# Performance work log

Measured on AMD Instinct MI355X. Metric: run time of the kernel, lower is better.

The kernel has to match this reference:

```python
import jax, jax.numpy as jnp
import numpy as np

N = 50000      # nodes
E = 400000     # edges
HID = 128      # hidden_size
L = 3          # num_att_layer
K = 9          # rbf_size
H = 4          # heads
C = HID // H   # out_channels per head (32)
G = 512        # graphs in batch
CUTOFF = 10.0


def _rbf(D):
    # ExponentialRBF: softplus(softplus_inverse(x)) == x, so centers/widths are the raw values
    centers = jnp.linspace(1.0, float(np.exp(-CUTOFF)), K)          # (K,)
    width = (0.5 / ((1.0 - np.exp(-CUTOFF)) / K)) ** 2              # scalar
    x = D / CUTOFF
    x3 = x ** 3
    x4 = x3 * x
    x5 = x4 * x
    cut = jnp.where(x < 1.0, 1.0 - 6.0 * x5 + 15.0 * x4 - 10.0 * x3, 0.0)
    return cut[:, None] * jnp.exp(-width * (jnp.exp(-D)[:, None] - centers) ** 2)  # (E,K)


def _ln(x, g, b):
    mu = jnp.mean(x, axis=-1, keepdims=True)
    var = jnp.var(x, axis=-1, keepdims=True)
    return (x - mu) / jnp.sqrt(var + 1e-5) * g + b


def _seg_softmax(logits, seg, n):
    # numerically stable softmax over edges grouped by target node
    m = jax.ops.segment_max(logits, seg, num_segments=n)
    e = jnp.exp(logits - m[seg])
    s = jax.ops.segment_sum(e, seg, num_segments=n)
    return e / s[seg]


def setup_inputs() -> dict:
    key = jax.random.key(0)
    ks = jax.random.split(key, 32)
    s = 1.0 / np.sqrt(HID)
    se = 1.0 / np.sqrt(K + 1)
    sb = 1.0 / np.sqrt(3 * HID)
    nrm = jax.random.normal
    inp = {
        "h": nrm(ks[0], (N, HID), jnp.float32),
        "pos": nrm(ks[1], (N, 3), jnp.float32) * 3.0,
        "edge_weight": jax.random.uniform(ks[2], (E,), jnp.float32),
        "Wq": nrm(ks[3], (L, HID, HID)) * s,   "bq": nrm(ks[4], (L, HID)) * 0.01,
        "Wk": nrm(ks[5], (L, HID, HID)) * s,   "bk": nrm(ks[6], (L, HID)) * 0.01,
        "Wv": nrm(ks[7], (L, HID, HID)) * s,   "bv": nrm(ks[8], (L, HID)) * 0.01,
        "We": nrm(ks[9], (L, K + 1, HID)) * se,
        "Wskip": nrm(ks[10], (L, HID, HID)) * s, "bskip": nrm(ks[11], (L, HID)) * 0.01,
        "Wbeta": nrm(ks[12], (L, 3 * HID, 1)) * sb,
        "Wffn1": nrm(ks[13], (L, HID, HID)) * s, "bffn1": nrm(ks[14], (L, HID)) * 0.01,
        "Wffn2": nrm(ks[15], (L, HID, HID)) * s, "bffn2": nrm(ks[16], (L, HID)) * 0.01,
        "Wffn3": nrm(ks[17], (L, HID, HID)) * s, "bffn3": nrm(ks[18], (L, HID)) * 0.01,
        "ln_g": jnp.ones((HID,), jnp.float32),
        "ln_b": jnp.zeros((HID,), jnp.float32),
        "Wo1": nrm(ks[19], (HID, HID)) * s, "bo1": nrm(ks[20], (HID,)) * 0.01,
        "Wo2": nrm(ks[21], (HID, 1)) * s,   "bo2": nrm(ks[22], (1,)) * 0.01,
        "edge_index": jax.random.randint(ks[23], (2, E), 0, N),
        "batch": jnp.sort(jax.random.randint(ks[24], (N,), 0, G)),
    }
    return inp


def reference(h, pos, edge_weight, Wq, bq, Wk, bk, Wv, bv, We, Wskip, bskip, Wbeta,
              Wffn1, bffn1, Wffn2, bffn2, Wffn3, bffn3, ln_g, ln_b, Wo1, bo1, Wo2, bo2,
              edge_index, batch):
    sp = jax.nn.softplus
    n = h.shape[0]
    src, dst = edge_index[0], edge_index[1]  # source j -> target i
    D = jnp.linalg.norm(pos[dst] - pos[src], axis=-1)              # (E,)
    efeat = jnp.concatenate([_rbf(D), edge_weight[:, None]], -1)   # (E, K+1)
    inv_sqrt_c = 1.0 / np.sqrt(C)

    for i in range(L):
        hn = _ln(h, ln_g, ln_b)
        q = (hn @ Wq[i] + bq[i]).reshape(n, H, C)
        k = (hn @ Wk[i] + bk[i]).reshape(n, H, C)
        v = (hn @ Wv[i] + bv[i]).reshape(n, H, C)
        ea = (efeat @ We[i]).reshape(-1, H, C)                     # (E,H,C)
        kj = k[src] + ea
        alpha = jnp.einsum('ehc,ehc->eh', q[dst], kj) * inv_sqrt_c  # (E,H)
        alpha = _seg_softmax(alpha, dst, n)
        # dropout p=0.5 is a no-op in eval mode
        msg = (v[src] + ea) * alpha[:, :, None]
        out = jax.ops.segment_sum(msg, dst, num_segments=n).reshape(n, H * C)
        x_r = hn @ Wskip[i] + bskip[i]
        beta = jax.nn.sigmoid(jnp.concatenate([out, x_r, out - x_r], -1) @ Wbeta[i])
        out = beta * x_r + (1.0 - beta) * out
        h = hn + sp(out)
        hn2 = _ln(h, ln_g, ln_b)
        f = sp(hn2 @ Wffn1[i] + bffn1[i])
        f = sp(f @ Wffn2[i] + bffn2[i])
        f = sp(f @ Wffn3[i] + bffn3[i])
        h = hn2 + f

    pooled = jax.ops.segment_sum(h, batch, num_segments=G)          # (G, HID)
    return sp(pooled @ Wo1 + bo1) @ Wo2 + bo2                       # (G, 1)
```

## Files before the change

### kernel.cpp

```cpp
#include <hip/hip_runtime.h>
#include <hip/hip_bf16.h>
#include <math.h>

#define HID 128
#define KRBF 9
#define NLAYER 3
#define QWCOLS 640

typedef __attribute__((ext_vector_type(8))) short bf16x8;
typedef __attribute__((ext_vector_type(4))) float f32x4;

__device__ __forceinline__ float sp_(float x){ return fmaxf(x,0.f) + log1pf(expf(-fabsf(x))); }
__device__ __forceinline__ float sigm_(float x){ return 1.f/(1.f+expf(-x)); }
__device__ __forceinline__ float b2f(short s){
  union{unsigned u; float f;} x; x.u = ((unsigned)(unsigned short)s)<<16; return x.f;
}
__device__ __forceinline__ short f2bs(float x){
  __hip_bfloat16 b = __float2bfloat16(x);
  return *reinterpret_cast<short*>(&b);
}
__device__ __forceinline__ float wsum64(float v){
  #pragma unroll
  for(int m=1;m<64;m<<=1) v += __shfl_xor(v,m,64);
  return v;
}
__device__ __forceinline__ float wsum16(float v){
  #pragma unroll
  for(int m=1;m<16;m<<=1) v += __shfl_xor(v,m,64);
  return v;
}
__device__ __forceinline__ int lb_(const int* __restrict__ a, int n, int key){
  int lo=0, hi=n;
  while(lo<hi){ int mid=(lo+hi)>>1; if(a[mid]<key) lo=mid+1; else hi=mid; }
  return lo;
}

__global__ void count_dst(const int* __restrict__ ei, int* __restrict__ counts, int E){
  int e = blockIdx.x*256+threadIdx.x;
  if(e<E) atomicAdd(&counts[ei[E+e]],1);
}
__global__ void scan1(const int* __restrict__ counts, int* __restrict__ tmp,
                      int* __restrict__ bsums, int N){
  __shared__ int lds[256];
  int t = threadIdx.x; int idx = blockIdx.x*256+t;
  int v = (idx<N)? counts[idx]:0;
  lds[t]=v; __syncthreads();
  for(int off=1;off<256;off<<=1){
    int x = (t>=off)? lds[t-off]:0;
    __syncthreads();
    lds[t]+=x; __syncthreads();
  }
  if(idx<N) tmp[idx]=lds[t];
  if(t==255) bsums[blockIdx.x]=lds[255];
}
__global__ void scan2(const int* __restrict__ bsums, int* __restrict__ boffs, int nb){
  __shared__ int lds[256];
  int t=threadIdx.x;
  int v = (t<nb)? bsums[t]:0;
  lds[t]=v; __syncthreads();
  for(int off=1;off<256;off<<=1){
    int x=(t>=off)?lds[t-off]:0;
    __syncthreads();
    lds[t]+=x; __syncthreads();
  }
  if(t<nb) boffs[t] = lds[t]-v;
}
__global__ void finalize_rs(const int* __restrict__ tmp, const int* __restrict__ boffs,
                            int* __restrict__ row_start, int N){
  int idx = blockIdx.x*256+threadIdx.x;
  if(idx<N) row_start[idx+1] = tmp[idx] + boffs[idx>>8];
  if(idx==0) row_start[0]=0;
}
__global__ void csr_scatter(const int* __restrict__ ei, const int* __restrict__ rowst,
                            int* __restrict__ counts2, int* __restrict__ csr, int E){
  int e = blockIdx.x*256+threadIdx.x;
  if(e>=E) return;
  int d = ei[E+e];
  int p = rowst[d] + atomicAdd(&counts2[d],1);
  csr[p] = e;
}
__global__ void sort_seg(const int* __restrict__ rowst, int* __restrict__ csr, int N){
  int n = blockIdx.x*256+threadIdx.x;
  if(n>=N) return;
  int lo=rowst[n], hi=rowst[n+1];
  for(int i=lo+1;i<hi;i++){
    int v=csr[i]; int j=i-1;
    while(j>=lo && csr[j]>v){ csr[j+1]=csr[j]; j--; }
    csr[j+1]=v;
  }
}
__global__ void edge_feat(const float* __restrict__ pos, const float* __restrict__ ew,
                          const int* __restrict__ ei, const int* __restrict__ csr,
                          float* __restrict__ efs, int* __restrict__ esrc, int E){
  int p = blockIdx.x*256 + threadIdx.x;
  if(p>=E) return;
  int e = csr[p];
  int s = ei[e], d = ei[E+e];
  float dx = pos[d*3+0]-pos[s*3+0];
  float dy = pos[d*3+1]-pos[s*3+1];
  float dz = pos[d*3+2]-pos[s*3+2];
  float D = sqrtf(dx*dx+dy*dy+dz*dz);
  float x = D*0.1f;
  float cut = 0.f;
  if(x < 1.f){ float x3=x*x*x, x4=x3*x, x5=x4*x; cut = 1.f - 6.f*x5 + 15.f*x4 - 10.f*x3; }
  float ed = expf(-D);
  const double e10 = 4.5399929762484854e-05;
  const float step  = (float)((e10 - 1.0)/8.0);
  const float width = (float)((4.5/(1.0-e10))*(4.5/(1.0-e10)));
  float r12[12];
  #pragma unroll
  for(int k=0;k<KRBF;k++){
    float c = 1.0f + k*step;
    float dd = ed - c;
    r12[k] = cut*expf(-width*dd*dd);
  }
  r12[9] = ew[e]; r12[10]=0.f; r12[11]=0.f;
  float* o = efs + (size_t)p*12;
  *(float4*)&o[0] = *(float4*)&r12[0];
  *(float4*)&o[4] = *(float4*)&r12[4];
  *(float4*)&o[8] = *(float4*)&r12[8];
  esrc[p] = s;
}

__global__ void pack_w(const float* __restrict__ Wq, const float* __restrict__ Wk,
                       const float* __restrict__ Wv, const float* __restrict__ Wsk,
                       const float* __restrict__ bq, const float* __restrict__ bk,
                       const float* __restrict__ bv, const float* __restrict__ bsk,
                       const float* __restrict__ We,
                       const float* __restrict__ W1, const float* __restrict__ W2,
                       const float* __restrict__ W3,
                       __hip_bfloat16* __restrict__ Wqkvs, float* __restrict__ bqkvs,
                       __hip_bfloat16* __restrict__ Wffn){
  int idx = blockIdx.x*256 + threadIdx.x;
  const int QT = NLAYER*QWCOLS*128;
  const int FT = NLAYER*3*128*128;
  const int BT = NLAYER*QWCOLS;
  if(idx < QT){
    int l = idx / (QWCOLS*128);
    int rem = idx - l*(QWCOLS*128);
    int colp = rem >> 7, k = rem & 127;
    int b = colp >> 7, p = colp & 127;
    int g = ((p&15)<<3) + (p>>4);
    int gcol = b*128 + g;
    float v = 0.f;
    if(gcol < 512){
      const float* src = (gcol<128)?Wq:((gcol<256)?Wk:((gcol<384)?Wv:Wsk));
      v = src[(size_t)l*16384 + k*128 + (gcol&127)];
    } else if(gcol < 552){
      int j = gcol-512; int h=j/10; int r=j-10*h;
      const float* wq = Wq + (size_t)l*16384 + k*128;
      const float* we = We + (size_t)l*1280 + r*128;
      float acc=0.f;
      #pragma unroll 8
      for(int c=32*h;c<32*h+32;c++) acc = fmaf(wq[c], we[c], acc);
      v = acc;
    }
    Wqkvs[idx] = __float2bfloat16(v);
  } else if(idx < QT+FT){
    int j = idx - QT;
    int k = j & 127; int colp = (j>>7)&127; int f = (j>>14)%3; int l = j/(3*16384);
    int g = ((colp&15)<<3) + (colp>>4);
    const float* src = (f==0)?W1:((f==1)?W2:W3);
    Wffn[j] = __float2bfloat16(src[(size_t)l*16384 + k*128 + g]);
  } else if(idx < QT+FT+BT){
    int j = idx - QT - FT;
    int l = j/QWCOLS; int col = j - l*QWCOLS;
    float v = 0.f;
    if(col<512){
      const float* src = (col<128)?bq:((col<256)?bk:((col<384)?bv:bsk));
      v = src[l*128 + (col&127)];
    } else if(col<552){
      int jj=col-512; int h=jj/10; int r=jj-10*h;
      const float* bqp = bq + l*128;
      const float* we = We + (size_t)l*1280 + r*128;
      float acc=0.f;
      for(int c=32*h;c<32*h+32;c++) acc = fmaf(bqp[c], we[c], acc);
      v = acc;
    }
    bqkvs[j] = v;
  }
}

__global__ void ln_node(const float* __restrict__ h, const float* __restrict__ g,
                        const float* __restrict__ b, __hip_bfloat16* __restrict__ hn, int N){
  int n = blockIdx.x*4 + (threadIdx.x>>6);
  if(n>=N) return;
  int lane = threadIdx.x & 63;
  int c = 2*lane;
  float2 v = *(const float2*)&h[(size_t)n*HID + c];
  float s1 = wsum64(v.x+v.y);
  float s2 = wsum64(v.x*v.x+v.y*v.y);
  float mu = s1*(1.f/HID);
  float var = s2*(1.f/HID) - mu*mu;
  float rs = rsqrtf(var + 1e-5f);
  __hip_bfloat162 o;
  o.x = __float2bfloat16((v.x-mu)*rs*g[c]   + b[c]);
  o.y = __float2bfloat16((v.y-mu)*rs*g[c+1] + b[c+1]);
  *(__hip_bfloat162*)&hn[(size_t)n*HID + c] = o;
}

__global__ __launch_bounds__(256) void gemm_qkvs(
    const __hip_bfloat16* __restrict__ A, const __hip_bfloat16* __restrict__ Wt,
    const float* __restrict__ bias,
    __hip_bfloat16* __restrict__ qsO, __hip_bfloat16* __restrict__ kvO,
    float* __restrict__ qwO, int N){
  __shared__ __hip_bfloat16 Ws[128][140];
  int row0 = blockIdx.y*128;
  int cb = blockIdx.x;
  int tid = threadIdx.x;
  {
    int chunk = tid&15, rbase = tid>>4;
    #pragma unroll
    for(int i=0;i<8;i++){
      int p = rbase + 16*i;
      *(float4*)&Ws[p][chunk*8] =
        *(const float4*)&Wt[(size_t)(cb*128+p)*128 + chunk*8];
    }
  }
  int lane = tid&63;
  int m0 = (tid>>6)*32;
  int ql = lane>>4, il = lane&15;
  bf16x8 af[2][4];
  #pragma unroll
  for(int mi=0;mi<2;mi++){
    int r = row0 + m0 + mi*16 + il;
    r = (r < N) ? r : (N-1);
    const __hip_bfloat16* ap = A + (size_t)r*128 + ql*8;
    #pragma unroll
    for(int kc=0;kc<4;kc++) af[mi][kc] = *(const bf16x8*)(ap + kc*32);
  }
  __syncthreads();
  f32x4 acc[2][8];
  #pragma unroll
  for(int mi=0;mi<2;mi++)
    #pragma unroll
    for(int nj=0;nj<8;nj++) acc[mi][nj] = (f32x4){0.f,0.f,0.f,0.f};
  #pragma unroll
  for(int kc=0;kc<4;kc++){
    #pragma unroll
    for(int nj=0;nj<8;nj++){
      bf16x8 bb = *(bf16x8*)&Ws[nj*16+il][kc*32+ql*8];
      #pragma unroll
      for(int mi=0;mi<2;mi++)
        acc[mi][nj] = __builtin_amdgcn_mfma_f32_16x16x32_bf16(af[mi][kc], bb, acc[mi][nj], 0,0,0);
    }
  }
  float bl8[8];
  {
    float4 b0 = *(const float4*)&bias[cb*128 + il*8];
    float4 b1 = *(const float4*)&bias[cb*128 + il*8 + 4];
    bl8[0]=b0.x; bl8[1]=b0.y; bl8[2]=b0.z; bl8[3]=b0.w;
    bl8[4]=b1.x; bl8[5]=b1.y; bl8[6]=b1.z; bl8[7]=b1.w;
  }
  #pragma unroll
  for(int mi=0;mi<2;mi++){
    #pragma unroll
    for(int r=0;r<4;r++){
      int rr = row0 + m0 + mi*16 + ql*4 + r;
      if(rr >= N) continue;
      if(cb < 4){
        bf16x8 o;
        #pragma unroll
        for(int nj=0;nj<8;nj++) o[nj] = f2bs(acc[mi][nj][r] + bl8[nj]);
        __hip_bfloat16* dst;
        if(cb==0)      dst = qsO + (size_t)rr*256 + il*8;
        else if(cb==1) dst = kvO + (size_t)rr*256 + il*8;
        else if(cb==2) dst = kvO + (size_t)rr*256 + 128 + il*8;
        else           dst = qsO + (size_t)rr*256 + 128 + il*8;
        *(bf16x8*)dst = o;
      } else if(il < 5){
        #pragma unroll
        for(int nj=0;nj<8;nj++){
          int g = il*8 + nj;
          int h = g/10, rb = g - 10*h;
          qwO[(size_t)rr*48 + h*12 + rb] = acc[mi][nj][r] + bl8[nj];
        }
      }
    }
  }
}

__global__ __launch_bounds__(256) void attn_fused4(
    const __hip_bfloat16* __restrict__ qs, const __hip_bfloat16* __restrict__ kvb,
    const float* __restrict__ qwb, const float* __restrict__ efs,
    const int* __restrict__ esrc, const float* __restrict__ WeL,
    const int* __restrict__ rowst, const __hip_bfloat16* __restrict__ hn,
    const float* __restrict__ Wb, const float* __restrict__ lng,
    const float* __restrict__ lnb, __hip_bfloat16* __restrict__ hn2, int N){
  int n = blockIdx.x*4 + (threadIdx.x>>6);
  if(n>=N) return;
  int lane = threadIdx.x & 63;
  int eg = lane>>4, sl = lane&15;
  int c8 = sl*8, hd = sl>>2;
  const __hip_bfloat16* rowq = qs + (size_t)n*256;
  float q8[8];
  {
    bf16x8 qv = *(const bf16x8*)&rowq[c8];
    #pragma unroll
    for(int j=0;j<8;j++) q8[j] = b2f(qv[j]);
  }
  const float* qwp = qwb + (size_t)n*48 + hd*12;
  float4 qa = *(const float4*)qwp;
  float4 qb = *(const float4*)(qwp+4);
  float2 qc = *(const float2*)(qwp+8);
  float QW[10] = {qa.x,qa.y,qa.z,qa.w,qb.x,qb.y,qb.z,qb.w,qc.x,qc.y};
  int lo = rowst[n], hi = rowst[n+1];
  float ssum = 0.f, a8[8], S[10];
  #pragma unroll
  for(int j=0;j<8;j++) a8[j]=0.f;
  #pragma unroll
  for(int r=0;r<10;r++) S[r]=0.f;
  int i = lo + eg;
  if(i < hi){
    int s = esrc[i];
    const __hip_bfloat16* kr = kvb + (size_t)s*256;
    bf16x8 kc = *(const bf16x8*)&kr[c8];
    bf16x8 vc = *(const bf16x8*)&kr[128 + c8];
    const float* ef = efs + (size_t)i*12;
    float4 e0 = *(const float4*)&ef[0];
    float4 e1 = *(const float4*)&ef[4];
    float2 e2 = *(const float2*)&ef[8];
    while(true){
      int inext = i + 4;
      bool more = inext < hi;
      bf16x8 kn = kc, vn = vc;
      float4 f0 = e0, f1 = e1; float2 f2 = e2;
      if(more){
        int s2 = esrc[inext];
        const __hip_bfloat16* kr2 = kvb + (size_t)s2*256;
        kn = *(const bf16x8*)&kr2[c8];
        vn = *(const bf16x8*)&kr2[128 + c8];
        const float* ef2 = efs + (size_t)inext*12;
        f0 = *(const float4*)&ef2[0];
        f1 = *(const float4*)&ef2[4];
        f2 = *(const float2*)&ef2[8];
      }
      float d = 0.f;
      #pragma unroll
      for(int j=0;j<8;j++) d = fmaf(q8[j], b2f(kc[j]), d);
      d += __shfl_xor(d,1,64); d += __shfl_xor(d,2,64);
      float lg = d;
      lg = fmaf(e0.x,QW[0],lg); lg = fmaf(e0.y,QW[1],lg);
      lg = fmaf(e0.z,QW[2],lg); lg = fmaf(e0.w,QW[3],lg);
      lg = fmaf(e1.x,QW[4],lg); lg = fmaf(e1.y,QW[5],lg);
      lg = fmaf(e1.z,QW[6],lg); lg = fmaf(e1.w,QW[7],lg);
      lg = fmaf(e2.x,QW[8],lg); lg = fmaf(e2.y,QW[9],lg);
      lg *= 0.17677669529663687f;
      lg = fminf(lg, 80.f);
      float w = __expf(lg);
      ssum += w;
      #pragma unroll
      for(int j=0;j<8;j++) a8[j] = fmaf(w, b2f(vc[j]), a8[j]);
      S[0]=fmaf(w,e0.x,S[0]); S[1]=fmaf(w,e0.y,S[1]); S[2]=fmaf(w,e0.z,S[2]);
      S[3]=fmaf(w,e0.w,S[3]); S[4]=fmaf(w,e1.x,S[4]); S[5]=fmaf(w,e1.y,S[5]);
      S[6]=fmaf(w,e1.z,S[6]); S[7]=fmaf(w,e1.w,S[7]); S[8]=fmaf(w,e2.x,S[8]);
      S[9]=fmaf(w,e2.y,S[9]);
      if(!more) break;
      kc = kn; vc = vn; e0 = f0; e1 = f1; e2 = f2;
      i = inext;
    }
  }
  #pragma unroll
  for(int m=16;m<64;m<<=1){
    ssum += __shfl_xor(ssum,m,64);
    #pragma unroll
    for(int j=0;j<8;j++) a8[j] += __shfl_xor(a8[j],m,64);
    #pragma unroll
    for(int r=0;r<10;r++) S[r] += __shfl_xor(S[r],m,64);
  }
  float inv = (hi>lo)? 1.f/ssum : 0.f;
  float o8[8];
  #pragma unroll
  for(int j=0;j<8;j++) o8[j]=a8[j];
  #pragma unroll
  for(int r=0;r<10;r++){
    float s=S[r];
    float4 wa = *(const float4*)&WeL[r*128+c8];
    float4 wb = *(const float4*)&WeL[r*128+c8+4];
    o8[0]=fmaf(s,wa.x,o8[0]); o8[1]=fmaf(s,wa.y,o8[1]);
    o8[2]=fmaf(s,wa.z,o8[2]); o8[3]=fmaf(s,wa.w,o8[3]);
    o8[4]=fmaf(s,wb.x,o8[4]); o8[5]=fmaf(s,wb.y,o8[5]);
    o8[6]=fmaf(s,wb.z,o8[6]); o8[7]=fmaf(s,wb.w,o8[7]);
  }
  #pragma unroll
  for(int j=0;j<8;j++) o8[j] *= inv;
  float xr8[8];
  {
    bf16x8 xv = *(const bf16x8*)&rowq[128 + c8];
    #pragma unroll
    for(int j=0;j<8;j++) xr8[j] = b2f(xv[j]);
  }
  float wb0[8], wb1[8], wb2[8];
  {
    float4 a0=*(const float4*)&Wb[c8],     a1=*(const float4*)&Wb[c8+4];
    float4 b0=*(const float4*)&Wb[128+c8], b1=*(const float4*)&Wb[128+c8+4];
    float4 c0=*(const float4*)&Wb[256+c8], c1=*(const float4*)&Wb[256+c8+4];
    wb0[0]=a0.x;wb0[1]=a0.y;wb0[2]=a0.z;wb0[3]=a0.w;wb0[4]=a1.x;wb0[5]=a1.y;wb0[6]=a1.z;wb0[7]=a1.w;
    wb1[0]=b0.x;wb1[1]=b0.y;wb1[2]=b0.z;wb1[3]=b0.w;wb1[4]=b1.x;wb1[5]=b1.y;wb1[6]=b1.z;wb1[7]=b1.w;
    wb2[0]=c0.x;wb2[1]=c0.y;wb2[2]=c0.z;wb2[3]=c0.w;wb2[4]=c1.x;wb2[5]=c1.y;wb2[6]=c1.z;wb2[7]=c1.w;
  }
  float pb = 0.f;
  #pragma unroll
  for(int j=0;j<8;j++)
    pb += o8[j]*wb0[j] + xr8[j]*wb1[j] + (o8[j]-xr8[j])*wb2[j];
  pb = wsum16(pb);
  float beta = sigm_(pb);
  float h8[8], s1=0.f, s2=0.f;
  {
    bf16x8 hv = *(const bf16x8*)&hn[(size_t)n*128 + c8];
    #pragma unroll
    for(int j=0;j<8;j++){
      float u = beta*xr8[j] + (1.f-beta)*o8[j];
      float x = b2f(hv[j]) + sp_(u);
      h8[j]=x; s1+=x; s2+=x*x;
    }
  }
  s1 = wsum16(s1); s2 = wsum16(s2);
  float mu = s1*(1.f/128.f);
  float var = s2*(1.f/128.f) - mu*mu;
  float rsg = rsqrtf(var + 1e-5f);
  if(eg==0){
    float4 g0=*(const float4*)&lng[c8], g1=*(const float4*)&lng[c8+4];
    float4 bb0=*(const float4*)&lnb[c8], bb1=*(const float4*)&lnb[c8+4];
    float g8[8]={g0.x,g0.y,g0.z,g0.w,g1.x,g1.y,g1.z,g1.w};
    float lb8[8]={bb0.x,bb0.y,bb0.z,bb0.w,bb1.x,bb1.y,bb1.z,bb1.w};
    bf16x8 o;
    #pragma unroll
    for(int j=0;j<8;j++) o[j] = f2bs((h8[j]-mu)*rsg*g8[j] + lb8[j]);
    *(bf16x8*)&hn2[(size_t)n*128 + c8] = o;
  }
}

__global__ __launch_bounds__(256) void ffn_fused(
    const __hip_bfloat16* __restrict__ hn2, const __hip_bfloat16* __restrict__ Wf,
    const float* __restrict__ b1, const float* __restrict__ b2,
    const float* __restrict__ b3, const float* __restrict__ lng,
    const float* __restrict__ lnb, float* __restrict__ hout,
    __hip_bfloat16* __restrict__ hnout, int N){
  __shared__ __hip_bfloat16 Ws[128][140];
  __shared__ __hip_bfloat16 inter[2][64][140];
  int row0 = blockIdx.x*64;
  int tid = threadIdx.x, lane = tid&63, wv = tid>>6;
  int ql = lane>>4, il = lane&15;
  int chunk = tid&15, rbase = tid>>4;

  auto stage = [&](const __hip_bfloat16* Wp){
    #pragma unroll
    for(int i=0;i<8;i++){
      int p = rbase + 16*i;
      *(float4*)&Ws[p][chunk*8] = *(const float4*)&Wp[(size_t)p*128 + chunk*8];
    }
  };
  auto loadbias = [&](const float* bp, float* bl8){
    float4 x0 = *(const float4*)&bp[il*8];
    float4 x1 = *(const float4*)&bp[il*8+4];
    bl8[0]=x0.x; bl8[1]=x0.y; bl8[2]=x0.z; bl8[3]=x0.w;
    bl8[4]=x1.x; bl8[5]=x1.y; bl8[6]=x1.z; bl8[7]=x1.w;
  };

  f32x4 acc[8];
  bf16x8 af[4];
  stage(Wf);
  {
    int r = row0 + wv*16 + il;
    r = (r<N)? r : (N-1);
    const __hip_bfloat16* ap = hn2 + (size_t)r*128 + ql*8;
    #pragma unroll
    for(int kc=0;kc<4;kc++) af[kc] = *(const bf16x8*)(ap + kc*32);
  }
  __syncthreads();
  #pragma unroll
  for(int nj=0;nj<8;nj++) acc[nj] = (f32x4){0.f,0.f,0.f,0.f};
  #pragma unroll
  for(int kc=0;kc<4;kc++)
    #pragma unroll
    for(int nj=0;nj<8;nj++){
      bf16x8 bb = *(bf16x8*)&Ws[nj*16+il][kc*32+ql*8];
      acc[nj] = __builtin_amdgcn_mfma_f32_16x16x32_bf16(af[kc], bb, acc[nj], 0,0,0);
    }
  {
    float bl8[8]; loadbias(b1, bl8);
    #pragma unroll
    for(int r=0;r<4;r++){
      int lr = wv*16 + ql*4 + r;
      bf16x8 o;
      #pragma unroll
      for(int nj=0;nj<8;nj++) o[nj] = f2bs(sp_(acc[nj][r] + bl8[nj]));
      *(bf16x8*)&inter[0][lr][il*8] = o;
    }
  }
  __syncthreads();
  stage(Wf + 16384);
  #pragma unroll
  for(int kc=0;kc<4;kc++) af[kc] = *(bf16x8*)&inter[0][wv*16+il][ql*8 + kc*32];
  __syncthreads();
  #pragma unroll
  for(int nj=0;nj<8;nj++) acc[nj] = (f32x4){0.f,0.f,0.f,0.f};
  #pragma unroll
  for(int kc=0;kc<4;kc++)
    #pragma unroll
    for(int nj=0;nj<8;nj++){
      bf16x8 bb = *(bf16x8*)&Ws[nj*16+il][kc*32+ql*8];
      acc[nj] = __builtin_amdgcn_mfma_f32_16x16x32_bf16(af[kc], bb, acc[nj], 0,0,0);
    }
  {
    float bl8[8]; loadbias(b2, bl8);
    #pragma unroll
    for(int r=0;r<4;r++){
      int lr = wv*16 + ql*4 + r;
      bf16x8 o;
      #pragma unroll
      for(int nj=0;nj<8;nj++) o[nj] = f2bs(sp_(acc[nj][r] + bl8[nj]));
      *(bf16x8*)&inter[1][lr][il*8] = o;
    }
  }
  __syncthreads();
  stage(Wf + 2*16384);
  #pragma unroll
  for(int kc=0;kc<4;kc++) af[kc] = *(bf16x8*)&inter[1][wv*16+il][ql*8 + kc*32];
  __syncthreads();
  #pragma unroll
  for(int nj=0;nj<8;nj++) acc[nj] = (f32x4){0.f,0.f,0.f,0.f};
  #pragma unroll
  for(int kc=0;kc<4;kc++)
    #pragma unroll
    for(int nj=0;nj<8;nj++){
      bf16x8 bb = *(bf16x8*)&Ws[nj*16+il][kc*32+ql*8];
      acc[nj] = __builtin_amdgcn_mfma_f32_16x16x32_bf16(af[kc], bb, acc[nj], 0,0,0);
    }
  {
    float bl8[8]; loadbias(b3, bl8);
    float lg8[8], lb8[8];
    loadbias(lng, lg8); loadbias(lnb, lb8);
    #pragma unroll
    for(int r=0;r<4;r++){
      int rr = row0 + wv*16 + ql*4 + r;
      if(rr >= N) continue;
      bf16x8 rv = *(const bf16x8*)&hn2[(size_t)rr*128 + il*8];
      float t8[8], s1=0.f, s2=0.f;
      #pragma unroll
      for(int nj=0;nj<8;nj++){
        float x = sp_(acc[nj][r] + bl8[nj]) + b2f(rv[nj]);
        t8[nj]=x; s1+=x; s2+=x*x;
      }
      s1 = wsum16(s1); s2 = wsum16(s2);
      float mu = s1*(1.f/128.f);
      float var = s2*(1.f/128.f) - mu*mu;
      float rsg = rsqrtf(var + 1e-5f);
      *(float4*)&hout[(size_t)rr*128 + il*8]     = make_float4(t8[0],t8[1],t8[2],t8[3]);
      *(float4*)&hout[(size_t)rr*128 + il*8 + 4] = make_float4(t8[4],t8[5],t8[6],t8[7]);
      bf16x8 o;
      #pragma unroll
      for(int nj=0;nj<8;nj++) o[nj] = f2bs((t8[nj]-mu)*rsg*lg8[nj] + lb8[nj]);
      *(bf16x8*)&hnout[(size_t)rr*128 + il*8] = o;
    }
  }
}

__global__ void pool_head(const float* __restrict__ h, const int* __restrict__ batch,
                          const float* __restrict__ Wo1, const float* __restrict__ bo1,
                          const float* __restrict__ Wo2, const float* __restrict__ bo2,
                          float* __restrict__ out, int N){
  int gid = blockIdx.x;
  int t = threadIdx.x;
  int lo = lb_(batch, N, gid), hi = lb_(batch, N, gid+1);
  __shared__ float pl[128];
  __shared__ float red[128];
  float s = 0.f;
  for(int i=lo;i<hi;i++) s += h[(size_t)i*HID + t];
  pl[t] = s;
  __syncthreads();
  float acc = bo1[t];
  for(int c=0;c<128;c++) acc = fmaf(pl[c], Wo1[c*HID+t], acc);
  red[t] = sp_(acc)*Wo2[t];
  __syncthreads();
  for(int off=64;off>0;off>>=1){
    if(t<off) red[t]+=red[t+off];
    __syncthreads();
  }
  if(t==0) out[gid] = red[0] + bo2[0];
}

extern "C" void kernel_launch(void* const* d_in, const int* in_sizes, int n_in,
                              void* d_out, int out_size, void* d_ws, size_t ws_size,
                              hipStream_t stream){
  const float* h_in = (const float*)d_in[0];
  const float* pos  = (const float*)d_in[1];
  const float* ew   = (const float*)d_in[2];
  const float* Wq = (const float*)d_in[3];  const float* bq = (const float*)d_in[4];
  const float* Wk = (const float*)d_in[5];  const float* bk = (const float*)d_in[6];
  const float* Wv = (const float*)d_in[7];  const float* bv = (const float*)d_in[8];
  const float* We = (const float*)d_in[9];
  const float* Wsk= (const float*)d_in[10]; const float* bsk=(const float*)d_in[11];
  const float* Wbeta=(const float*)d_in[12];
  const float* W1=(const float*)d_in[13]; const float* b1=(const float*)d_in[14];
  const float* W2=(const float*)d_in[15]; const float* b2=(const float*)d_in[16];
  const float* W3=(const float*)d_in[17]; const float* b3=(const float*)d_in[18];
  const float* lng=(const float*)d_in[19]; const float* lnb=(const float*)d_in[20];
  const float* Wo1=(const float*)d_in[21]; const float* bo1=(const float*)d_in[22];
  const float* Wo2=(const float*)d_in[23]; const float* bo2=(const float*)d_in[24];
  const int* ei    = (const int*)d_in[25];
  const int* batch = (const int*)d_in[26];
  int N = in_sizes[0]/HID;
  int E = in_sizes[2];
  int G = out_size;
  float* out = (float*)d_out;

  char* ws = (char*)d_ws;
  size_t off=0;
  auto alloc=[&](size_t bytes)->char*{
    char* p = ws + off;
    off = (off + bytes + 255) & ~(size_t)255;
    return p;
  };
  float* efs   =(float*)alloc((size_t)E*12*4);
  int* esrc    =(int*)  alloc((size_t)E*4);
  int* csr     =(int*)  alloc((size_t)E*4);
  int* counts  =(int*)  alloc((size_t)N*4);
  int* counts2 =(int*)  alloc((size_t)N*4);
  int* rowst   =(int*)  alloc((size_t)(N+1)*4);
  int* tmp     =(int*)  alloc((size_t)N*4);
  int* bsums   =(int*)  alloc(256*4);
  int* boffs   =(int*)  alloc(256*4);
  __hip_bfloat16* hn   =(__hip_bfloat16*)alloc((size_t)N*HID*2);
  __hip_bfloat16* hn2  =(__hip_bfloat16*)alloc((size_t)N*HID*2);
  __hip_bfloat16* qsb  =(__hip_bfloat16*)alloc((size_t)N*256*2);
  __hip_bfloat16* kvb  =(__hip_bfloat16*)alloc((size_t)N*256*2);
  float* qwb   =(float*)alloc((size_t)N*48*4);
  float* hcur  =(float*)alloc((size_t)N*HID*4);
  __hip_bfloat16* Wqkvs_t =(__hip_bfloat16*)alloc((size_t)NLAYER*QWCOLS*128*2);
  __hip_bfloat16* Wffn_t  =(__hip_bfloat16*)alloc((size_t)NLAYER*3*128*128*2);
  float* bqkvs =(float*)alloc((size_t)NLAYER*QWCOLS*4);

  int ebl = (E+255)/256;
  int nb  = (N+255)/256;
  int nwb = (N+3)/4;
  int nrb128 = (N+127)/128;
  int nrb64  = (N+63)/64;
  dim3 gqkvs(QWCOLS/128, nrb128);

  hipMemsetAsync(counts, 0, (size_t)N*4, stream);
  hipMemsetAsync(counts2,0, (size_t)N*4, stream);
  count_dst<<<ebl,256,0,stream>>>(ei,counts,E);
  scan1<<<nb,256,0,stream>>>(counts,tmp,bsums,N);
  scan2<<<1,256,0,stream>>>(bsums,boffs,nb);
  finalize_rs<<<nb,256,0,stream>>>(tmp,boffs,rowst,N);
  csr_scatter<<<ebl,256,0,stream>>>(ei,rowst,counts2,csr,E);
  sort_seg<<<nb,256,0,stream>>>(rowst,csr,N);
  edge_feat<<<ebl,256,0,stream>>>(pos,ew,ei,csr,efs,esrc,E);
  {
    int tot = NLAYER*QWCOLS*128 + NLAYER*3*128*128 + NLAYER*QWCOLS;
    pack_w<<<(tot+255)/256,256,0,stream>>>(Wq,Wk,Wv,Wsk,bq,bk,bv,bsk,We,W1,W2,W3,
                                           Wqkvs_t,bqkvs,Wffn_t);
  }

  ln_node<<<nwb,256,0,stream>>>(h_in,lng,lnb,hn,N);
  for(int l=0;l<NLAYER;l++){
    const float* We_l = We + (size_t)l*(KRBF+1)*HID;
    const float* Wb_l = Wbeta + (size_t)l*3*HID;
    const float* b1_l = b1 + (size_t)l*HID;
    const float* b2_l = b2 + (size_t)l*HID;
    const float* b3_l = b3 + (size_t)l*HID;

    gemm_qkvs<<<gqkvs,256,0,stream>>>(hn, Wqkvs_t + (size_t)l*QWCOLS*128,
                                      bqkvs + l*QWCOLS, qsb, kvb, qwb, N);
    attn_fused4<<<nwb,256,0,stream>>>(qsb,kvb,qwb,efs,esrc,We_l,rowst,hn,
                                      Wb_l,lng,lnb,hn2,N);
    ffn_fused<<<nrb64,256,0,stream>>>(hn2, Wffn_t + (size_t)l*3*16384,
                                      b1_l,b2_l,b3_l,lng,lnb,hcur,hn,N);
  }
  pool_head<<<G,128,0,stream>>>(hcur,batch,Wo1,bo1,Wo2,bo2,out,N);
}
```

Baseline: 966.6 us.

## Assign one 16-lane group per node, degree-sorted, and retune LDS padding

The attention kernel now maps each destination node to a 16-lane group, where it was a 64-lane wave split into four edge groups. This removes the cross-group shuffle reduction and the idle lanes on low-degree nodes. Nodes are processed in degree-sorted order via a counting-sort permutation built once in preprocessing, so groups in a wave see similar edge counts and diverge less. The LDS row padding in the GEMM kernels changes from 140 to 142. Per-node edge processing is now serial within a group, so latency hiding on long rows relies on more concurrent groups, and the permuted node order scatters the q/hn reads and writes.

```diff
diff --git a/kernel.cpp b/kernel.cpp
--- a/kernel.cpp
+++ b/kernel.cpp
@@ -6,6 +6,7 @@
 #define KRBF 9
 #define NLAYER 3
 #define QWCOLS 640
+#define WPAD 142
 
 typedef __attribute__((ext_vector_type(8))) short bf16x8;
 typedef __attribute__((ext_vector_type(4))) float f32x4;
@@ -120,6 +121,31 @@
   *(float4*)&o[4] = *(float4*)&r12[4];
   *(float4*)&o[8] = *(float4*)&r12[8];
   esrc[p] = s;
+}
+
+__global__ void deg_hist(const int* __restrict__ counts, int* __restrict__ dhist, int N){
+  int n = blockIdx.x*256+threadIdx.x;
+  if(n<N) atomicAdd(&dhist[min(counts[n],255)],1);
+}
+__global__ void deg_scan(const int* __restrict__ dhist, int* __restrict__ dstart){
+  __shared__ int lds[256];
+  int t=threadIdx.x;
+  int v = dhist[t];
+  lds[t]=v; __syncthreads();
+  for(int off=1;off<256;off<<=1){
+    int x=(t>=off)?lds[t-off]:0;
+    __syncthreads();
+    lds[t]+=x; __syncthreads();
+  }
+  dstart[t] = lds[t]-v;
+}
+__global__ void deg_scatter(const int* __restrict__ counts, const int* __restrict__ dstart,
+                            int* __restrict__ dcur, int* __restrict__ perm, int N){
+  int n = blockIdx.x*256+threadIdx.x;
+  if(n>=N) return;
+  int d = min(counts[n],255);
+  int p = dstart[d] + atomicAdd(&dcur[d],1);
+  perm[p] = n;
 }
 
 __global__ void pack_w(const float* __restrict__ Wq, const float* __restrict__ Wk,
@@ -204,7 +230,7 @@
     const float* __restrict__ bias,
     __hip_bfloat16* __restrict__ qsO, __hip_bfloat16* __restrict__ kvO,
     float* __restrict__ qwO, int N){
-  __shared__ __hip_bfloat16 Ws[128][140];
+  __shared__ __hip_bfloat16 Ws[128][WPAD];
   int row0 = blockIdx.y*128;
   int cb = blockIdx.x;
   int tid = threadIdx.x;
@@ -280,24 +306,25 @@
   }
 }
 
-__global__ __launch_bounds__(256) void attn_fused4(
+__global__ __launch_bounds__(256) void attn_fused5(
     const __hip_bfloat16* __restrict__ qs, const __hip_bfloat16* __restrict__ kvb,
     const float* __restrict__ qwb, const float* __restrict__ efs,
     const int* __restrict__ esrc, const float* __restrict__ WeL,
-    const int* __restrict__ rowst, const __hip_bfloat16* __restrict__ hn,
-    const float* __restrict__ Wb, const float* __restrict__ lng,
-    const float* __restrict__ lnb, __hip_bfloat16* __restrict__ hn2, int N){
-  int n = blockIdx.x*4 + (threadIdx.x>>6);
-  if(n>=N) return;
-  int lane = threadIdx.x & 63;
-  int eg = lane>>4, sl = lane&15;
+    const int* __restrict__ rowst, const int* __restrict__ perm,
+    const __hip_bfloat16* __restrict__ hn, const float* __restrict__ Wb,
+    const float* __restrict__ lng, const float* __restrict__ lnb,
+    __hip_bfloat16* __restrict__ hn2, int N){
+  int j = blockIdx.x*16 + (threadIdx.x>>4);
+  if(j>=N) return;
+  int n = perm[j];
+  int sl = threadIdx.x & 15;
   int c8 = sl*8, hd = sl>>2;
   const __hip_bfloat16* rowq = qs + (size_t)n*256;
   float q8[8];
   {
     bf16x8 qv = *(const bf16x8*)&rowq[c8];
     #pragma unroll
-    for(int j=0;j<8;j++) q8[j] = b2f(qv[j]);
+    for(int jj=0;jj<8;jj++) q8[jj] = b2f(qv[jj]);
   }
   const float* qwp = qwb + (size_t)n*48 + hd*12;
   float4 qa = *(const float4*)qwp;
@@ -307,10 +334,10 @@
   int lo = rowst[n], hi = rowst[n+1];
   float ssum = 0.f, a8[8], S[10];
   #pragma unroll
-  for(int j=0;j<8;j++) a8[j]=0.f;
+  for(int jj=0;jj<8;jj++) a8[jj]=0.f;
   #pragma unroll
   for(int r=0;r<10;r++) S[r]=0.f;
-  int i = lo + eg;
+  int i = lo;
   if(i < hi){
     int s = esrc[i];
     const __hip_bfloat16* kr = kvb + (size_t)s*256;
@@ -321,7 +348,7 @@
     float4 e1 = *(const float4*)&ef[4];
     float2 e2 = *(const float2*)&ef[8];
     while(true){
-      int inext = i + 4;
+      int inext = i + 1;
       bool more = inext < hi;
       bf16x8 kn = kc, vn = vc;
       float4 f0 = e0, f1 = e1; float2 f2 = e2;
@@ -337,7 +364,7 @@
       }
       float d = 0.f;
       #pragma unroll
-      for(int j=0;j<8;j++) d = fmaf(q8[j], b2f(kc[j]), d);
+      for(int jj=0;jj<8;jj++) d = fmaf(q8[jj], b2f(kc[jj]), d);
       d += __shfl_xor(d,1,64); d += __shfl_xor(d,2,64);
       float lg = d;
       lg = fmaf(e0.x,QW[0],lg); lg = fmaf(e0.y,QW[1],lg);
@@ -350,7 +377,7 @@
       float w = __expf(lg);
       ssum += w;
       #pragma unroll
-      for(int j=0;j<8;j++) a8[j] = fmaf(w, b2f(vc[j]), a8[j]);
+      for(int jj=0;jj<8;jj++) a8[jj] = fmaf(w, b2f(vc[jj]), a8[jj]);
       S[0]=fmaf(w,e0.x,S[0]); S[1]=fmaf(w,e0.y,S[1]); S[2]=fmaf(w,e0.z,S[2]);
       S[3]=fmaf(w,e0.w,S[3]); S[4]=fmaf(w,e1.x,S[4]); S[5]=fmaf(w,e1.y,S[5]);
       S[6]=fmaf(w,e1.z,S[6]); S[7]=fmaf(w,e1.w,S[7]); S[8]=fmaf(w,e2.x,S[8]);
@@ -360,18 +387,10 @@
       i = inext;
     }
   }
-  #pragma unroll
-  for(int m=16;m<64;m<<=1){
-    ssum += __shfl_xor(ssum,m,64);
-    #pragma unroll
-    for(int j=0;j<8;j++) a8[j] += __shfl_xor(a8[j],m,64);
-    #pragma unroll
-    for(int r=0;r<10;r++) S[r] += __shfl_xor(S[r],m,64);
-  }
   float inv = (hi>lo)? 1.f/ssum : 0.f;
   float o8[8];
   #pragma unroll
-  for(int j=0;j<8;j++) o8[j]=a8[j];
+  for(int jj=0;jj<8;jj++) o8[jj]=a8[jj];
   #pragma unroll
   for(int r=0;r<10;r++){
     float s=S[r];
@@ -383,50 +402,49 @@
     o8[6]=fmaf(s,wb.z,o8[6]); o8[7]=fmaf(s,wb.w,o8[7]);
   }
   #pragma unroll
-  for(int j=0;j<8;j++) o8[j] *= inv;
+  for(int jj=0;jj<8;jj++) o8[jj] *= inv;
   float xr8[8];
   {
     bf16x8 xv = *(const bf16x8*)&rowq[128 + c8];
     #pragma unroll
-    for(int j=0;j<8;j++) xr8[j] = b2f(xv[j]);
-  }
-  float wb0[8], wb1[8], wb2[8];
+    for(int jj=0;jj<8;jj++) xr8[jj] = b2f(xv[jj]);
+  }
+  float pb = 0.f;
   {
     float4 a0=*(const float4*)&Wb[c8],     a1=*(const float4*)&Wb[c8+4];
     float4 b0=*(const float4*)&Wb[128+c8], b1=*(const float4*)&Wb[128+c8+4];
     float4 c0=*(const float4*)&Wb[256+c8], c1=*(const float4*)&Wb[256+c8+4];
-    wb0[0]=a0.x;wb0[1]=a0.y;wb0[2]=a0.z;wb0[3]=a0.w;wb0[4]=a1.x;wb0[5]=a1.y;wb0[6]=a1.z;wb0[7]=a1.w;
-    wb1[0]=b0.x;wb1[1]=b0.y;wb1[2]=b0.z;wb1[3]=b0.w;wb1[4]=b1.x;wb1[5]=b1.y;wb1[6]=b1.z;wb1[7]=b1.w;
-    wb2[0]=c0.x;wb2[1]=c0.y;wb2[2]=c0.z;wb2[3]=c0.w;wb2[4]=c1.x;wb2[5]=c1.y;wb2[6]=c1.z;wb2[7]=c1.w;
-  }
-  float pb = 0.f;
-  #pragma unroll
-  for(int j=0;j<8;j++)
-    pb += o8[j]*wb0[j] + xr8[j]*wb1[j] + (o8[j]-xr8[j])*wb2[j];
+    float wb0[8]={a0.x,a0.y,a0.z,a0.w,a1.x,a1.y,a1.z,a1.w};
+    float wb1[8]={b0.x,b0.y,b0.z,b0.w,b1.x,b1.y,b1.z,b1.w};
+    float wb2[8]={c0.x,c0.y,c0.z,c0.w,c1.x,c1.y,c1.z,c1.w};
+    #pragma unroll
+    for(int jj=0;jj<8;jj++)
+      pb += o8[jj]*wb0[jj] + xr8[jj]*wb1[jj] + (o8[jj]-xr8[jj])*wb2[jj];
+  }
   pb = wsum16(pb);
   float beta = sigm_(pb);
   float h8[8], s1=0.f, s2=0.f;
   {
     bf16x8 hv = *(const bf16x8*)&hn[(size_t)n*128 + c8];
     #pragma unroll
-    for(int j=0;j<8;j++){
-      float u = beta*xr8[j] + (1.f-beta)*o8[j];
-      float x = b2f(hv[j]) + sp_(u);
-      h8[j]=x; s1+=x; s2+=x*x;
+    for(int jj=0;jj<8;jj++){
+      float u = beta*xr8[jj] + (1.f-beta)*o8[jj];
+      float x = b2f(hv[jj]) + sp_(u);
+      h8[jj]=x; s1+=x; s2+=x*x;
     }
   }
   s1 = wsum16(s1); s2 = wsum16(s2);
   float mu = s1*(1.f/128.f);
   float var = s2*(1.f/128.f) - mu*mu;
   float rsg = rsqrtf(var + 1e-5f);
-  if(eg==0){
+  {
     float4 g0=*(const float4*)&lng[c8], g1=*(const float4*)&lng[c8+4];
     float4 bb0=*(const float4*)&lnb[c8], bb1=*(const float4*)&lnb[c8+4];
     float g8[8]={g0.x,g0.y,g0.z,g0.w,g1.x,g1.y,g1.z,g1.w};
     float lb8[8]={bb0.x,bb0.y,bb0.z,bb0.w,bb1.x,bb1.y,bb1.z,bb1.w};
     bf16x8 o;
     #pragma unroll
-    for(int j=0;j<8;j++) o[j] = f2bs((h8[j]-mu)*rsg*g8[j] + lb8[j]);
+    for(int jj=0;jj<8;jj++) o[jj] = f2bs((h8[jj]-mu)*rsg*g8[jj] + lb8[jj]);
     *(bf16x8*)&hn2[(size_t)n*128 + c8] = o;
   }
 }
@@ -437,8 +455,8 @@
     const float* __restrict__ b3, const float* __restrict__ lng,
     const float* __restrict__ lnb, float* __restrict__ hout,
     __hip_bfloat16* __restrict__ hnout, int N){
-  __shared__ __hip_bfloat16 Ws[128][140];
-  __shared__ __hip_bfloat16 inter[2][64][140];
+  __shared__ __hip_bfloat16 Ws[128][WPAD];
+  __shared__ __hip_bfloat16 inter[2][64][WPAD];
   int row0 = blockIdx.x*64;
   int tid = threadIdx.x, lane = tid&63, wv = tid>>6;
   int ql = lane>>4, il = lane&15;
@@ -622,6 +640,10 @@
   int* tmp     =(int*)  alloc((size_t)N*4);
   int* bsums   =(int*)  alloc(256*4);
   int* boffs   =(int*)  alloc(256*4);
+  int* perm    =(int*)  alloc((size_t)N*4);
+  int* dhist   =(int*)  alloc(256*4);
+  int* dstart  =(int*)  alloc(256*4);
+  int* dcur    =(int*)  alloc(256*4);
   __hip_bfloat16* hn   =(__hip_bfloat16*)alloc((size_t)N*HID*2);
   __hip_bfloat16* hn2  =(__hip_bfloat16*)alloc((size_t)N*HID*2);
   __hip_bfloat16* qsb  =(__hip_bfloat16*)alloc((size_t)N*256*2);
@@ -635,12 +657,15 @@
   int ebl = (E+255)/256;
   int nb  = (N+255)/256;
   int nwb = (N+3)/4;
+  int ngb = (N+15)/16;
   int nrb128 = (N+127)/128;
   int nrb64  = (N+63)/64;
   dim3 gqkvs(QWCOLS/128, nrb128);
 
   hipMemsetAsync(counts, 0, (size_t)N*4, stream);
   hipMemsetAsync(counts2,0, (size_t)N*4, stream);
+  hipMemsetAsync(dhist,  0, 256*4, stream);
+  hipMemsetAsync(dcur,   0, 256*4, stream);
   count_dst<<<ebl,256,0,stream>>>(ei,counts,E);
   scan1<<<nb,256,0,stream>>>(counts,tmp,bsums,N);
   scan2<<<1,256,0,stream>>>(bsums,boffs,nb);
@@ -648,6 +673,9 @@
   csr_scatter<<<ebl,256,0,stream>>>(ei,rowst,counts2,csr,E);
   sort_seg<<<nb,256,0,stream>>>(rowst,csr,N);
   edge_feat<<<ebl,256,0,stream>>>(pos,ew,ei,csr,efs,esrc,E);
+  deg_hist<<<nb,256,0,stream>>>(counts,dhist,N);
+  deg_scan<<<1,256,0,stream>>>(dhist,dstart);
+  deg_scatter<<<nb,256,0,stream>>>(counts,dstart,dcur,perm,N);
   {
     int tot = NLAYER*QWCOLS*128 + NLAYER*3*128*128 + NLAYER*QWCOLS;
     pack_w<<<(tot+255)/256,256,0,stream>>>(Wq,Wk,Wv,Wsk,bq,bk,bv,bsk,We,W1,W2,W3,
@@ -664,7 +692,7 @@
 
     gemm_qkvs<<<gqkvs,256,0,stream>>>(hn, Wqkvs_t + (size_t)l*QWCOLS*128,
                                       bqkvs + l*QWCOLS, qsb, kvb, qwb, N);
-    attn_fused4<<<nwb,256,0,stream>>>(qsb,kvb,qwb,efs,esrc,We_l,rowst,hn,
+    attn_fused5<<<ngb,256,0,stream>>>(qsb,kvb,qwb,efs,esrc,We_l,rowst,perm,hn,
                                       Wb_l,lng,lnb,hn2,N);
     ffn_fused<<<nrb64,256,0,stream>>>(hn2, Wffn_t + (size_t)l*3*16384,
                                       b1_l,b2_l,b3_l,lng,lnb,hcur,hn,N);
```

Measured after the change: 1.579 ms. 1.63x slower.

## Pre-swizzle weights into MFMA fragment order and defer attention reductions

Applied to the files above, without the earlier changes.

Weight packing now writes the QKVS and FFN weight matrices directly in per-lane MFMA B-fragment order. The GEMM kernels can then stage them with flat contiguous copies and read each fragment as one linear 16-byte load from shared memory with no padding, which removes strided LDS reads and possible bank conflicts. The attention kernel applies the edge-feature weight projection before the cross-lane shuffle reduction, so only 8 outputs are reduced instead of 8 plus 10 S values. The beta weight loads are also scoped more tightly to lower register pressure. The packing index math is more complex and must exactly match the consumer layout.

```diff
diff --git a/kernel.cpp b/kernel.cpp
--- a/kernel.cpp
+++ b/kernel.cpp
@@ -5,7 +5,7 @@
 #define HID 128
 #define KRBF 9
 #define NLAYER 3
-#define QWCOLS 640
+#define IPAD 136
 
 typedef __attribute__((ext_vector_type(8))) short bf16x8;
 typedef __attribute__((ext_vector_type(4))) float f32x4;
@@ -132,22 +132,24 @@
                        __hip_bfloat16* __restrict__ Wqkvs, float* __restrict__ bqkvs,
                        __hip_bfloat16* __restrict__ Wffn){
   int idx = blockIdx.x*256 + threadIdx.x;
-  const int QT = NLAYER*QWCOLS*128;
-  const int FT = NLAYER*3*128*128;
-  const int BT = NLAYER*QWCOLS;
+  const int QT = NLAYER*5*16384;
+  const int FT = NLAYER*3*16384;
+  const int BT = NLAYER*640;
   if(idx < QT){
-    int l = idx / (QWCOLS*128);
-    int rem = idx - l*(QWCOLS*128);
-    int colp = rem >> 7, k = rem & 127;
-    int b = colp >> 7, p = colp & 127;
-    int g = ((p&15)<<3) + (p>>4);
-    int gcol = b*128 + g;
+    int l = idx / (5*16384);
+    int rem = idx - l*(5*16384);
+    int cb = rem >> 14;
+    int t = rem & 16383;
+    int j = t&7; int lane = (t>>3)&63; int blk = t>>9;
+    int kc = blk>>3, nj = blk&7, ql = lane>>4, il = lane&15;
+    int k = kc*32 + ql*8 + j;
+    int gcol = cb*128 + il*8 + nj;
     float v = 0.f;
     if(gcol < 512){
       const float* src = (gcol<128)?Wq:((gcol<256)?Wk:((gcol<384)?Wv:Wsk));
       v = src[(size_t)l*16384 + k*128 + (gcol&127)];
     } else if(gcol < 552){
-      int j = gcol-512; int h=j/10; int r=j-10*h;
+      int jj = gcol-512; int h=jj/10; int r=jj-10*h;
       const float* wq = Wq + (size_t)l*16384 + k*128;
       const float* we = We + (size_t)l*1280 + r*128;
       float acc=0.f;
@@ -157,14 +159,20 @@
     }
     Wqkvs[idx] = __float2bfloat16(v);
   } else if(idx < QT+FT){
-    int j = idx - QT;
-    int k = j & 127; int colp = (j>>7)&127; int f = (j>>14)%3; int l = j/(3*16384);
-    int g = ((colp&15)<<3) + (colp>>4);
+    int r0 = idx - QT;
+    int l = r0 / (3*16384);
+    int rem = r0 - l*(3*16384);
+    int f = rem >> 14;
+    int t = rem & 16383;
+    int j = t&7; int lane = (t>>3)&63; int blk = t>>9;
+    int kc = blk>>3, nj = blk&7, ql = lane>>4, il = lane&15;
+    int k = kc*32 + ql*8 + j;
+    int gcol = il*8 + nj;
     const float* src = (f==0)?W1:((f==1)?W2:W3);
-    Wffn[j] = __float2bfloat16(src[(size_t)l*16384 + k*128 + g]);
+    Wffn[r0] = __float2bfloat16(src[(size_t)l*16384 + k*128 + gcol]);
   } else if(idx < QT+FT+BT){
     int j = idx - QT - FT;
-    int l = j/QWCOLS; int col = j - l*QWCOLS;
+    int l = j/640; int col = j - l*640;
     float v = 0.f;
     if(col<512){
       const float* src = (col<128)?bq:((col<256)?bk:((col<384)?bv:bsk));
@@ -204,17 +212,16 @@
     const float* __restrict__ bias,
     __hip_bfloat16* __restrict__ qsO, __hip_bfloat16* __restrict__ kvO,
     float* __restrict__ qwO, int N){
-  __shared__ __hip_bfloat16 Ws[128][140];
+  __shared__ __hip_bfloat16 WsF[16384];
   int row0 = blockIdx.y*128;
   int cb = blockIdx.x;
   int tid = threadIdx.x;
   {
-    int chunk = tid&15, rbase = tid>>4;
+    const __hip_bfloat16* Wp = Wt + (size_t)cb*16384;
     #pragma unroll
     for(int i=0;i<8;i++){
-      int p = rbase + 16*i;
-      *(float4*)&Ws[p][chunk*8] =
-        *(const float4*)&Wt[(size_t)(cb*128+p)*128 + chunk*8];
+      int o = (tid + 256*i)*8;
+      *(float4*)&WsF[o] = *(const float4*)&Wp[o];
     }
   }
   int lane = tid&63;
@@ -239,7 +246,7 @@
   for(int kc=0;kc<4;kc++){
     #pragma unroll
     for(int nj=0;nj<8;nj++){
-      bf16x8 bb = *(bf16x8*)&Ws[nj*16+il][kc*32+ql*8];
+      bf16x8 bb = *(bf16x8*)&WsF[((kc*8+nj)*64 + lane)*8];
       #pragma unroll
       for(int mi=0;mi<2;mi++)
         acc[mi][nj] = __builtin_amdgcn_mfma_f32_16x16x32_bf16(af[mi][kc], bb, acc[mi][nj], 0,0,0);
@@ -360,15 +367,6 @@
       i = inext;
     }
   }
-  #pragma unroll
-  for(int m=16;m<64;m<<=1){
-    ssum += __shfl_xor(ssum,m,64);
-    #pragma unroll
-    for(int j=0;j<8;j++) a8[j] += __shfl_xor(a8[j],m,64);
-    #pragma unroll
-    for(int r=0;r<10;r++) S[r] += __shfl_xor(S[r],m,64);
-  }
-  float inv = (hi>lo)? 1.f/ssum : 0.f;
   float o8[8];
   #pragma unroll
   for(int j=0;j<8;j++) o8[j]=a8[j];
@@ -383,6 +381,13 @@
     o8[6]=fmaf(s,wb.z,o8[6]); o8[7]=fmaf(s,wb.w,o8[7]);
   }
   #pragma unroll
+  for(int m=16;m<64;m<<=1){
+    ssum += __shfl_xor(ssum,m,64);
+    #pragma unroll
+    for(int j=0;j<8;j++) o8[j] += __shfl_xor(o8[j],m,64);
+  }
+  float inv = (hi>lo)? 1.f/ssum : 0.f;
+  #pragma unroll
   for(int j=0;j<8;j++) o8[j] *= inv;
   float xr8[8];
   {
@@ -390,19 +395,18 @@
     #pragma unroll
     for(int j=0;j<8;j++) xr8[j] = b2f(xv[j]);
   }
-  float wb0[8], wb1[8], wb2[8];
+  float pb = 0.f;
   {
     float4 a0=*(const float4*)&Wb[c8],     a1=*(const float4*)&Wb[c8+4];
     float4 b0=*(const float4*)&Wb[128+c8], b1=*(const float4*)&Wb[128+c8+4];
     float4 c0=*(const float4*)&Wb[256+c8], c1=*(const float4*)&Wb[256+c8+4];
-    wb0[0]=a0.x;wb0[1]=a0.y;wb0[2]=a0.z;wb0[3]=a0.w;wb0[4]=a1.x;wb0[5]=a1.y;wb0[6]=a1.z;wb0[7]=a1.w;
-    wb1[0]=b0.x;wb1[1]=b0.y;wb1[2]=b0.z;wb1[3]=b0.w;wb1[4]=b1.x;wb1[5]=b1.y;wb1[6]=b1.z;wb1[7]=b1.w;
-    wb2[0]=c0.x;wb2[1]=c0.y;wb2[2]=c0.z;wb2[3]=c0.w;wb2[4]=c1.x;wb2[5]=c1.y;wb2[6]=c1.z;wb2[7]=c1.w;
-  }
-  float pb = 0.f;
-  #pragma unroll
-  for(int j=0;j<8;j++)
-    pb += o8[j]*wb0[j] + xr8[j]*wb1[j] + (o8[j]-xr8[j])*wb2[j];
+    float wb0[8]={a0.x,a0.y,a0.z,a0.w,a1.x,a1.y,a1.z,a1.w};
+    float wb1[8]={b0.x,b0.y,b0.z,b0.w,b1.x,b1.y,b1.z,b1.w};
+    float wb2[8]={c0.x,c0.y,c0.z,c0.w,c1.x,c1.y,c1.z,c1.w};
+    #pragma unroll
+    for(int j=0;j<8;j++)
+      pb += o8[j]*wb0[j] + xr8[j]*wb1[j] + (o8[j]-xr8[j])*wb2[j];
+  }
   pb = wsum16(pb);
   float beta = sigm_(pb);
   float h8[8], s1=0.f, s2=0.f;
@@ -437,18 +441,17 @@
     const float* __restrict__ b3, const float* __restrict__ lng,
     const float* __restrict__ lnb, float* __restrict__ hout,
     __hip_bfloat16* __restrict__ hnout, int N){
-  __shared__ __hip_bfloat16 Ws[128][140];
-  __shared__ __hip_bfloat16 inter[2][64][140];
+  __shared__ __hip_bfloat16 WsF[16384];
+  __shared__ __hip_bfloat16 inter[2][64][IPAD];
   int row0 = blockIdx.x*64;
   int tid = threadIdx.x, lane = tid&63, wv = tid>>6;
   int ql = lane>>4, il = lane&15;
-  int chunk = tid&15, rbase = tid>>4;
 
   auto stage = [&](const __hip_bfloat16* Wp){
     #pragma unroll
     for(int i=0;i<8;i++){
-      int p = rbase + 16*i;
-      *(float4*)&Ws[p][chunk*8] = *(const float4*)&Wp[(size_t)p*128 + chunk*8];
+      int o = (tid + 256*i)*8;
+      *(float4*)&WsF[o] = *(const float4*)&Wp[o];
     }
   };
   auto loadbias = [&](const float* bp, float* bl8){
@@ -475,7 +478,7 @@
   for(int kc=0;kc<4;kc++)
     #pragma unroll
     for(int nj=0;nj<8;nj++){
-      bf16x8 bb = *(bf16x8*)&Ws[nj*16+il][kc*32+ql*8];
+      bf16x8 bb = *(bf16x8*)&WsF[((kc*8+nj)*64 + lane)*8];
       acc[nj] = __builtin_amdgcn_mfma_f32_16x16x32_bf16(af[kc], bb, acc[nj], 0,0,0);
     }
   {
@@ -500,7 +503,7 @@
   for(int kc=0;kc<4;kc++)
     #pragma unroll
     for(int nj=0;nj<8;nj++){
-      bf16x8 bb = *(bf16x8*)&Ws[nj*16+il][kc*32+ql*8];
+      bf16x8 bb = *(bf16x8*)&WsF[((kc*8+nj)*64 + lane)*8];
       acc[nj] = __builtin_amdgcn_mfma_f32_16x16x32_bf16(af[kc], bb, acc[nj], 0,0,0);
     }
   {
@@ -525,7 +528,7 @@
   for(int kc=0;kc<4;kc++)
     #pragma unroll
     for(int nj=0;nj<8;nj++){
-      bf16x8 bb = *(bf16x8*)&Ws[nj*16+il][kc*32+ql*8];
+      bf16x8 bb = *(bf16x8*)&WsF[((kc*8+nj)*64 + lane)*8];
       acc[nj] = __builtin_amdgcn_mfma_f32_16x16x32_bf16(af[kc], bb, acc[nj], 0,0,0);
     }
   {
@@ -628,16 +631,16 @@
   __hip_bfloat16* kvb  =(__hip_bfloat16*)alloc((size_t)N*256*2);
   float* qwb   =(float*)alloc((size_t)N*48*4);
   float* hcur  =(float*)alloc((size_t)N*HID*4);
-  __hip_bfloat16* Wqkvs_t =(__hip_bfloat16*)alloc((size_t)NLAYER*QWCOLS*128*2);
-  __hip_bfloat16* Wffn_t  =(__hip_bfloat16*)alloc((size_t)NLAYER*3*128*128*2);
-  float* bqkvs =(float*)alloc((size_t)NLAYER*QWCOLS*4);
+  __hip_bfloat16* Wqkvs_t =(__hip_bfloat16*)alloc((size_t)NLAYER*5*16384*2);
+  __hip_bfloat16* Wffn_t  =(__hip_bfloat16*)alloc((size_t)NLAYER*3*16384*2);
+  float* bqkvs =(float*)alloc((size_t)NLAYER*640*4);
 
   int ebl = (E+255)/256;
   int nb  = (N+255)/256;
   int nwb = (N+3)/4;
   int nrb128 = (N+127)/128;
   int nrb64  = (N+63)/64;
-  dim3 gqkvs(QWCOLS/128, nrb128);
+  dim3 gqkvs(5, nrb128);
 
   hipMemsetAsync(counts, 0, (size_t)N*4, stream);
   hipMemsetAsync(counts2,0, (size_t)N*4, stream);
@@ -649,7 +652,7 @@
   sort_seg<<<nb,256,0,stream>>>(rowst,csr,N);
   edge_feat<<<ebl,256,0,stream>>>(pos,ew,ei,csr,efs,esrc,E);
   {
-    int tot = NLAYER*QWCOLS*128 + NLAYER*3*128*128 + NLAYER*QWCOLS;
+    int tot = NLAYER*5*16384 + NLAYER*3*16384 + NLAYER*640;
     pack_w<<<(tot+255)/256,256,0,stream>>>(Wq,Wk,Wv,Wsk,bq,bk,bv,bsk,We,W1,W2,W3,
                                            Wqkvs_t,bqkvs,Wffn_t);
   }
@@ -662,8 +665,8 @@
     const float* b2_l = b2 + (size_t)l*HID;
     const float* b3_l = b3 + (size_t)l*HID;
 
-    gemm_qkvs<<<gqkvs,256,0,stream>>>(hn, Wqkvs_t + (size_t)l*QWCOLS*128,
-                                      bqkvs + l*QWCOLS, qsb, kvb, qwb, N);
+    gemm_qkvs<<<gqkvs,256,0,stream>>>(hn, Wqkvs_t + (size_t)l*5*16384,
+                                      bqkvs + l*640, qsb, kvb, qwb, N);
     attn_fused4<<<nwb,256,0,stream>>>(qsb,kvb,qwb,efs,esrc,We_l,rowst,hn,
                                       Wb_l,lng,lnb,hn2,N);
     ffn_fused<<<nrb64,256,0,stream>>>(hn2, Wffn_t + (size_t)l*3*16384,
```

After: 926.7 us. -4.1%, faster.
